# Kernel tuning notes

Hardware: AMD Instinct MI355X
Metric: run time of the kernel (lower is better)

Reference implementation:

```python
import jax, jax.numpy as jnp
import numpy as np

B, T1, T2, D, H, NL, DFF, NC = 4, 128, 128, 512, 4, 4, 2048, 5
SQRT2 = 1.4142135623730951


def _ln(x, w, b, eps=1e-12):
    m = jnp.mean(x, -1, keepdims=True)
    v = jnp.mean((x - m) ** 2, -1, keepdims=True)
    return w * (x - m) / jnp.sqrt(v + eps) + b


def _gelu(x):  # erf-based gelu, as in source
    return x * 0.5 * (1.0 + jax.lax.erf(x / SQRT2))


def _mha(x, wq, bq, wk, bk, wv, bv, wo, bo):
    b, t, d = x.shape
    dk = d // H
    q = (x @ wq + bq).reshape(b, t, H, dk).transpose(0, 2, 1, 3)
    k = (x @ wk + bk).reshape(b, t, H, dk).transpose(0, 2, 1, 3)
    v = (x @ wv + bv).reshape(b, t, H, dk).transpose(0, 2, 1, 3)
    p = jax.nn.softmax(jnp.einsum('bhqd,bhkd->bhqk', q, k) / jnp.sqrt(jnp.float32(dk)), -1)
    o = jnp.einsum('bhqk,bhkd->bhqd', p, v).transpose(0, 2, 1, 3).reshape(b, t, d)
    return o @ wo + bo


def _encode(x, pos_emb, pe_w, pe_b, Wq, bq, Wk, bk, Wv, bv, Wo, bo,
            ff1_w, ff1_b, ff2_w, ff2_b, lnin_w, lnin_b, lnout_w, lnout_b):
    t = x.shape[1]
    x = _ln(x + pos_emb[:t], pe_w, pe_b)  # PositionalEncoding (dropout=0 eval)
    for i in range(Wq.shape[0]):  # EncoderLayer x NL
        x = x + _mha(x, Wq[i], bq[i], Wk[i], bk[i], Wv[i], bv[i], Wo[i], bo[i])
        h = _ln(x, lnin_w[i], lnin_b[i])
        x = x + (_gelu(h @ ff1_w[i] + ff1_b[i]) @ ff2_w[i] + ff2_b[i])
        x = _ln(x, lnout_w[i], lnout_b[i])
    return x


def _forward(q_emb, a_emb, qa_relation, aq_relation, concept_emb, pos_emb, pe_w, pe_b,
             Wq, bq, Wk, bk, Wv, bv, Wo, bo, ff1_w, ff1_b, ff2_w, ff2_b,
             lnin_w, lnin_b, lnout_w, lnout_b, sim_Wq, sim_bq, sim_Wk, sim_bk, cls_w, cls_b):
    enc = lambda x: _encode(x, pos_emb, pe_w, pe_b, Wq, bq, Wk, bk, Wv, bv, Wo, bo,
                            ff1_w, ff1_b, ff2_w, ff2_b, lnin_w, lnin_b, lnout_w, lnout_b)
    qe = enc(q_emb)   # [B,T1,D]
    ae = enc(a_emb)   # [B,T2,D]
    # ConceptEncoding: relation one-hots -> concept embedding mix
    hL = qa_relation @ concept_emb   # [B,T1,T2,D]
    hR = aq_relation @ concept_emb   # [B,T2,T1,D]
    # SimAttn: note source uses fwK for BOTH key and value, so v == k exactly
    q = qe @ sim_Wq + sim_bq
    k = ae @ sim_Wk + sim_bk
    kR = jnp.transpose(k[:, :, None, :] + hR, (0, 2, 1, 3))  # [B,T1,T2,D]
    scores = jnp.sum((q[:, :, None, :] + hL) * kR, axis=-1)   # [B,T1,T2]
    p = jax.nn.softmax(scores, -1)
    # sharpening branch (default sharpening=True): re-softmax the attention probs
    p = jnp.clip(jax.nn.softmax(1000.0 * p, -1), 0.0, 1.0)
    # value path: v + hR transposed == kR since v == k
    x = jnp.einsum('bts,btsd->btd', p, kR)                    # [B,T1,D]
    return jnp.mean(x, 1) @ cls_w + cls_b                     # [B,3]


def setup_inputs() -> dict:
    key = jax.random.key(0)
    rk = lambda i: jax.random.fold_in(key, i)
    w = lambda i, shape: 0.02 * jax.random.normal(rk(i), shape, jnp.float32)
    z = lambda shape: jnp.zeros(shape, jnp.float32)
    o = lambda shape: jnp.ones(shape, jnp.float32)
    return {
        'q_emb': jax.random.normal(rk(0), (B, T1, D), jnp.float32),
        'a_emb': jax.random.normal(rk(1), (B, T2, D), jnp.float32),
        'qa_relation': jax.random.uniform(rk(2), (B, T1, T2, NC), jnp.float32),
        'aq_relation': jax.random.uniform(rk(3), (B, T2, T1, NC), jnp.float32),
        'concept_emb': w(4, (NC, D)),
        'pos_emb': w(5, (512, D)),
        'pe_w': o((D,)), 'pe_b': z((D,)),
        'Wq': w(6, (NL, D, D)), 'bq': z((NL, D)),
        'Wk': w(7, (NL, D, D)), 'bk': z((NL, D)),
        'Wv': w(8, (NL, D, D)), 'bv': z((NL, D)),
        'Wo': w(9, (NL, D, D)), 'bo': z((NL, D)),
        'ff1_w': w(10, (NL, D, DFF)), 'ff1_b': z((NL, DFF)),
        'ff2_w': w(11, (NL, DFF, D)), 'ff2_b': z((NL, D)),
        'lnin_w': o((NL, D)), 'lnin_b': z((NL, D)),
        'lnout_w': o((NL, D)), 'lnout_b': z((NL, D)),
        'sim_Wq': w(12, (D, D)), 'sim_bq': z((D,)),
        'sim_Wk': w(13, (D, D)), 'sim_bk': z((D,)),
        'cls_w': w(14, (D, 3)), 'cls_b': z((3,)),
    }


def reference(q_emb, a_emb, qa_relation, aq_relation, concept_emb, pos_emb, pe_w, pe_b,
              Wq, bq, Wk, bk, Wv, bv, Wo, bo, ff1_w, ff1_b, ff2_w, ff2_b,
              lnin_w, lnin_b, lnout_w, lnout_b, sim_Wq, sim_bq, sim_Wk, sim_bk, cls_w, cls_b):
    return _forward(q_emb, a_emb, qa_relation, aq_relation, concept_emb, pos_emb, pe_w, pe_b,
                    Wq, bq, Wk, bk, Wv, bv, Wo, bo, ff1_w, ff1_b, ff2_w, ff2_b,
                    lnin_w, lnin_b, lnout_w, lnout_b, sim_Wq, sim_bq, sim_Wk, sim_bk, cls_w, cls_b)
```

## Files before the change

kernel.cpp:

```cpp
#include <hip/hip_runtime.h>
#include <hip/hip_bf16.h>
#include <math.h>

typedef unsigned short u16;
typedef __attribute__((ext_vector_type(8))) short bf16x8;
typedef __attribute__((ext_vector_type(4))) float f32x4;

__device__ __forceinline__ float ldin(const void* p, size_t i, int isbf) {
  if (isbf) return __bfloat162float(((const __hip_bfloat16*)p)[i]);
  return ((const float*)p)[i];
}
__device__ __forceinline__ float bfu(u16 u) { return __builtin_bit_cast(float, (unsigned)u << 16); }
__device__ __forceinline__ u16 f2bf(float x) {
  unsigned u = __builtin_bit_cast(unsigned, x);
  unsigned r = u + 0x7FFFu + ((u >> 16) & 1u);
  return (u16)(r >> 16);
}

__device__ __forceinline__ float wave_sum(float v) {
#pragma unroll
  for (int o = 32; o > 0; o >>= 1) v += __shfl_down(v, o);
  return v;
}

__device__ __forceinline__ float block_sum(float v, float* sbuf) {
  int lane = threadIdx.x & 63;
  int wid = threadIdx.x >> 6;
#pragma unroll
  for (int o = 32; o > 0; o >>= 1) v += __shfl_down(v, o);
  __syncthreads();
  if (lane == 0) sbuf[wid] = v;
  __syncthreads();
  int nw = blockDim.x >> 6;
  if (wid == 0) {
    float r = (lane < nw) ? sbuf[lane] : 0.f;
#pragma unroll
    for (int o = 4; o > 0; o >>= 1) r += __shfl_down(r, o);
    if (lane == 0) sbuf[0] = r;
  }
  __syncthreads();
  return sbuf[0];
}

__device__ __forceinline__ float block_max(float v, float* sbuf) {
  int lane = threadIdx.x & 63;
  int wid = threadIdx.x >> 6;
#pragma unroll
  for (int o = 32; o > 0; o >>= 1) v = fmaxf(v, __shfl_down(v, o));
  __syncthreads();
  if (lane == 0) sbuf[wid] = v;
  __syncthreads();
  int nw = blockDim.x >> 6;
  if (wid == 0) {
    float r = (lane < nw) ? sbuf[lane] : -INFINITY;
#pragma unroll
    for (int o = 4; o > 0; o >>= 1) r = fmaxf(r, __shfl_down(r, o));
    if (lane == 0) sbuf[0] = r;
  }
  __syncthreads();
  return sbuf[0];
}

__global__ void flag_kernel(const void* pe_w, int* flag) {
  if (threadIdx.x == 0 && blockIdx.x == 0)
    *flag = (((const unsigned short*)pe_w)[0] != 0) ? 1 : 0;
}

__global__ void init_kernel(const void* pe_w, int* flag, float* Pbar, float* pabar) {
  int t = threadIdx.x;
  if (t == 0) *flag = (((const unsigned short*)pe_w)[0] != 0) ? 1 : 0;
  if (t < 512) Pbar[t] = 0.f;
  if (t < 20) pabar[t] = 0.f;
}


__global__ __launch_bounds__(256) void convT2(
    const void* __restrict__ S0, const void* __restrict__ S1,
    const void* __restrict__ S2, const void* __restrict__ S3,
    size_t srcStride, int K, int N, u16* __restrict__ Dh, u16* __restrict__ Dl,
    size_t layerStride, size_t tensorStride, int tmask, int lshift,
    const int* __restrict__ dflag) {
  const int isbf = *dflag;
  int z = blockIdx.z;
  int t = z & tmask, l = z >> lshift;
  const void* S = (t == 0) ? S0 : ((t == 1) ? S1 : ((t == 2) ? S2 : S3));
  size_t soff = (size_t)l * srcStride;
  size_t doff = (size_t)l * layerStride + (size_t)t * tensorStride;
  int n0 = blockIdx.x * 32, k0 = blockIdx.y * 32;
  __shared__ float tt[32][33];
  int tx = threadIdx.x & 31, ty = threadIdx.x >> 5;
#pragma unroll
  for (int j = 0; j < 4; ++j) {
    int r = ty + j * 8;
    tt[r][tx] = ldin(S, soff + (size_t)(k0 + r) * N + n0 + tx, isbf);
  }
  __syncthreads();
#pragma unroll
  for (int j = 0; j < 4; ++j) {
    int r = ty + j * 8;
    float v = tt[tx][r];
    u16 h = f2bf(v);
    u16 lo = f2bf(v - bfu(h));
    size_t o = doff + (size_t)(n0 + r) * K + k0 + tx;
    Dh[o] = h;
    Dl[o] = lo;
  }
}

__global__ __launch_bounds__(256) void gemm_hl(
    const u16* __restrict__ Ahp, const u16* __restrict__ Alp, int lda,
    const u16* __restrict__ Whp, const u16* __restrict__ Wlp, int ldw,
    const void* __restrict__ b0, const void* __restrict__ b1, const void* __restrict__ b2,
    size_t bo0, size_t bo1, size_t bo2, int bshift,
    float* __restrict__ C, u16* __restrict__ Chp, u16* __restrict__ Clp,
    u16* __restrict__ Vh, u16* __restrict__ Vl, int ldc,
    int K, int act, int mode, int ysplit, size_t wrowoff1,
    const int* __restrict__ dflag) {
  const int isbf = *dflag;
  __shared__ __align__(16) u16 sAh[64][72];
  __shared__ __align__(16) u16 sAl[64][72];
  __shared__ __align__(16) u16 sBh[64][72];
  __shared__ __align__(16) u16 sBl[64][72];

  int tid = threadIdx.x;
  int by = blockIdx.y;
  int row0 = by * 64, col0 = blockIdx.x * 64;
  int rsplit = (by >= ysplit);
  size_t wrow0 = (size_t)col0 + (rsplit ? wrowoff1 : 0);
  int Ksub = K / (int)gridDim.z;
  int kstart = (int)blockIdx.z * Ksub;
  int addbias = (blockIdx.z == 0);

  int wid = tid >> 6, lane = tid & 63, quad = lane >> 4, lm = lane & 15;
  int mrow = (wid & 1) * 32, ncol = (wid >> 1) * 32;

  f32x4 acc[2][2] = {};

  int sr = tid >> 2, sc = (tid & 3) * 16;

  for (int k0 = kstart; k0 < kstart + Ksub; k0 += 64) {
    const u16* p;
    p = Ahp + (size_t)(row0 + sr) * lda + k0 + sc;
    uint4 a0 = *(const uint4*)p, a1 = *(const uint4*)(p + 8);
    p = Alp + (size_t)(row0 + sr) * lda + k0 + sc;
    uint4 a2 = *(const uint4*)p, a3 = *(const uint4*)(p + 8);
    p = Whp + (wrow0 + sr) * (size_t)ldw + k0 + sc;
    uint4 w0 = *(const uint4*)p, w1 = *(const uint4*)(p + 8);
    p = Wlp + (wrow0 + sr) * (size_t)ldw + k0 + sc;
    uint4 w2 = *(const uint4*)p, w3 = *(const uint4*)(p + 8);
    __syncthreads();
    *(uint4*)&sAh[sr][sc] = a0; *(uint4*)&sAh[sr][sc + 8] = a1;
    *(uint4*)&sAl[sr][sc] = a2; *(uint4*)&sAl[sr][sc + 8] = a3;
    *(uint4*)&sBh[sr][sc] = w0; *(uint4*)&sBh[sr][sc + 8] = w1;
    *(uint4*)&sBl[sr][sc] = w2; *(uint4*)&sBl[sr][sc + 8] = w3;
    __syncthreads();
#pragma unroll
    for (int ks = 0; ks < 2; ++ks) {
      bf16x8 ah[2], al[2], wh[2], wl[2];
#pragma unroll
      for (int mi = 0; mi < 2; ++mi) {
        ah[mi] = *(const bf16x8*)&sAh[mrow + mi * 16 + lm][ks * 32 + quad * 8];
        al[mi] = *(const bf16x8*)&sAl[mrow + mi * 16 + lm][ks * 32 + quad * 8];
      }
#pragma unroll
      for (int ni = 0; ni < 2; ++ni) {
        wh[ni] = *(const bf16x8*)&sBh[ncol + ni * 16 + lm][ks * 32 + quad * 8];
        wl[ni] = *(const bf16x8*)&sBl[ncol + ni * 16 + lm][ks * 32 + quad * 8];
      }
#pragma unroll
      for (int mi = 0; mi < 2; ++mi)
#pragma unroll
        for (int ni = 0; ni < 2; ++ni) {
          acc[mi][ni] = __builtin_amdgcn_mfma_f32_16x16x32_bf16(ah[mi], wh[ni], acc[mi][ni], 0, 0, 0);
          acc[mi][ni] = __builtin_amdgcn_mfma_f32_16x16x32_bf16(al[mi], wh[ni], acc[mi][ni], 0, 0, 0);
          acc[mi][ni] = __builtin_amdgcn_mfma_f32_16x16x32_bf16(ah[mi], wl[ni], acc[mi][ni], 0, 0, 0);
        }
    }
  }
#pragma unroll
  for (int mi = 0; mi < 2; ++mi) {
#pragma unroll
    for (int ni = 0; ni < 2; ++ni) {
      int colg = col0 + ncol + ni * 16 + lm;
      const void* bp; size_t bo;
      if (rsplit) { bp = b1; bo = bo1 + colg; }
      else {
        int seg = colg >> bshift;
        bp = (seg == 0) ? b0 : ((seg == 1) ? b1 : b2);
        bo = (seg == 0) ? bo0 : ((seg == 1) ? bo1 : bo2);
        bo += (size_t)colg - ((size_t)seg << bshift);
      }
      float bv = addbias ? ldin(bp, bo, isbf) : 0.f;
#pragma unroll
      for (int r = 0; r < 4; ++r) {
        int rowg = row0 + mrow + mi * 16 + quad * 4 + r;
        float v = acc[mi][ni][r] + bv;
        if (act) v = v * 0.5f * (1.f + erff(v * 0.70710678118654752f));
        if (mode == 3 && colg >= 1024) {
          int gg = rowg >> 7;
          size_t o = ((size_t)(gg * 512) + (colg - 1024)) * 128 + (rowg & 127);
          u16 hh = f2bf(v); Vh[o] = hh; Vl[o] = f2bf(v - bfu(hh));
        } else {
          size_t o = (size_t)rowg * ldc + colg;
          if (mode == 0) C[o] = v;
          else if (mode == 1) atomicAdd(&C[o], v);
          else { u16 hh = f2bf(v); Chp[o] = hh; Clp[o] = f2bf(v - bfu(hh)); }
        }
      }
    }
  }
}

__global__ __launch_bounds__(256) void attn_mfma(
    const u16* __restrict__ Qh, const u16* __restrict__ Ql,
    const u16* __restrict__ Vth, const u16* __restrict__ Vtl,
    u16* __restrict__ Oh, u16* __restrict__ Ol) {
  int tq = blockIdx.x & 3;
  int h = (blockIdx.x >> 2) & 3;
  int g = blockIdx.x >> 4;
  int tid = threadIdx.x;
  int w = tid >> 6, lane = tid & 63, quad = lane >> 4, lm = lane & 15;
  __shared__ float S[32][132];

  f32x4 sacc[2][2] = {};
#pragma unroll
  for (int ks = 0; ks < 4; ++ks) {
    bf16x8 qh[2], ql[2];
#pragma unroll
    for (int mi = 0; mi < 2; ++mi) {
      size_t qi = (size_t)(g * 128 + tq * 32 + mi * 16 + lm) * 1536 + h * 128 + ks * 32 + quad * 8;
      qh[mi] = *(const bf16x8*)(Qh + qi);
      ql[mi] = *(const bf16x8*)(Ql + qi);
    }
#pragma unroll
    for (int ni = 0; ni < 2; ++ni) {
      size_t kix = (size_t)(g * 128 + w * 32 + ni * 16 + lm) * 1536 + 512 + h * 128 + ks * 32 + quad * 8;
      bf16x8 kh = *(const bf16x8*)(Qh + kix);
      bf16x8 kl = *(const bf16x8*)(Ql + kix);
#pragma unroll
      for (int mi = 0; mi < 2; ++mi) {
        sacc[mi][ni] = __builtin_amdgcn_mfma_f32_16x16x32_bf16(qh[mi], kh, sacc[mi][ni], 0, 0, 0);
        sacc[mi][ni] = __builtin_amdgcn_mfma_f32_16x16x32_bf16(ql[mi], kh, sacc[mi][ni], 0, 0, 0);
        sacc[mi][ni] = __builtin_amdgcn_mfma_f32_16x16x32_bf16(qh[mi], kl, sacc[mi][ni], 0, 0, 0);
      }
    }
  }
  const float scale = 0.08838834764831845f;
#pragma unroll
  for (int mi = 0; mi < 2; ++mi)
#pragma unroll
    for (int ni = 0; ni < 2; ++ni)
#pragma unroll
      for (int r = 0; r < 4; ++r)
        S[mi * 16 + quad * 4 + r][w * 32 + ni * 16 + lm] = sacc[mi][ni][r] * scale;
  __syncthreads();

  {
    int row = tid >> 3, j = tid & 7;
    float* sp = &S[row][j * 16];
// ... 98 lines not shown
  u16 h1 = f2bf(r1); oh[o1] = h1; ol[o1] = f2bf(r1 - bfu(h1));
}

__global__ __launch_bounds__(256) void ln2(
    const float* __restrict__ in, float* __restrict__ outf,
    u16* __restrict__ oh, u16* __restrict__ ol,
    const void* __restrict__ w, const void* __restrict__ b, size_t wboff,
    const int* __restrict__ dflag) {
  const int isbf = *dflag;
  const int D = 512;
  int row = blockIdx.x;
  __shared__ float sbuf[8];
  int i0 = threadIdx.x, i1 = threadIdx.x + 256;
  float v0 = in[(size_t)row * D + i0];
  float v1 = in[(size_t)row * D + i1];
  float mean = block_sum(v0 + v1, sbuf) / 512.f;
  float d0 = v0 - mean, d1 = v1 - mean;
  float var = block_sum(d0 * d0 + d1 * d1, sbuf) / 512.f;
  float inv = 1.0f / sqrtf(var + 1e-12f);
  float r0 = ldin(w, wboff + i0, isbf) * d0 * inv + ldin(b, wboff + i0, isbf);
  float r1 = ldin(w, wboff + i1, isbf) * d1 * inv + ldin(b, wboff + i1, isbf);
  size_t o0 = (size_t)row * D + i0, o1 = (size_t)row * D + i1;
  if (outf) { outf[o0] = r0; outf[o1] = r1; }
  u16 h0 = f2bf(r0); oh[o0] = h0; ol[o0] = f2bf(r0 - bfu(h0));
  u16 h1 = f2bf(r1); oh[o1] = h1; ol[o1] = f2bf(r1 - bfu(h1));
}

__global__ __launch_bounds__(64) void projgram(const float* __restrict__ qkb,
                                               const void* __restrict__ ce,
                                               float* __restrict__ ck, float* __restrict__ G,
                                               const int* __restrict__ dflag) {
  const int isbf = *dflag;
  if (blockIdx.x < 1024) {
    int row = blockIdx.x;
#pragma unroll
    for (int c = 0; c < 5; ++c) {
      float acc = 0.f;
      for (int d = threadIdx.x; d < 512; d += 64)
        acc = fmaf(qkb[(size_t)row * 512 + d], ldin(ce, (size_t)c * 512 + d, isbf), acc);
      acc = wave_sum(acc);
      if (threadIdx.x == 0) ck[row * 5 + c] = acc;
    }
  } else {
    int i = blockIdx.x - 1024;
    int c = i / 5, c2 = i % 5;
    float acc = 0.f;
    for (int d = threadIdx.x; d < 512; d += 64)
      acc = fmaf(ldin(ce, (size_t)c * 512 + d, isbf), ldin(ce, (size_t)c2 * 512 + d, isbf), acc);
    acc = wave_sum(acc);
    if (threadIdx.x == 0) G[i] = acc;
  }
}

__global__ __launch_bounds__(128) void scores_acc(
    const float* __restrict__ qkb, const void* __restrict__ qa, const void* __restrict__ aq,
    const float* __restrict__ ck, const float* __restrict__ G,
    float* __restrict__ Pbar, float* __restrict__ pabar, const int* __restrict__ dflag) {
  const int isbf = *dflag;
  const int T1 = 128, T2 = 128, D = 512, NC = 5;
  int t = blockIdx.x & 127;
  int b = blockIdx.x >> 7;
  int s = threadIdx.x;
  const float* q = qkb;
  const float* k = qkb + (size_t)512 * 512;
  __shared__ float qs[512];
  __shared__ float Gs[25];
  __shared__ float qcs[5];
  __shared__ float sbuf[8];
  for (int i = threadIdx.x; i < D; i += 128) qs[i] = q[(size_t)(b * T1 + t) * D + i];
  if (threadIdx.x < NC * NC) Gs[threadIdx.x] = G[threadIdx.x];
  if (threadIdx.x < NC) qcs[threadIdx.x] = ck[(size_t)(b * T1 + t) * NC + threadIdx.x];
  __syncthreads();
  const float* krow = k + (size_t)(b * T2 + s) * D;
  float sc = 0.f;
#pragma unroll 4
  for (int d = 0; d < 512; d += 4) {
    float4 kv4 = *(const float4*)(krow + d);
    sc = fmaf(qs[d], kv4.x, sc);
    sc = fmaf(qs[d + 1], kv4.y, sc);
    sc = fmaf(qs[d + 2], kv4.z, sc);
    sc = fmaf(qs[d + 3], kv4.w, sc);
  }
  float qav[5], aqv[5];
#pragma unroll
  for (int c = 0; c < 5; ++c) {
    qav[c] = ldin(qa, (size_t)((b * T1 + t) * T2 + s) * NC + c, isbf);
    aqv[c] = ldin(aq, (size_t)((b * T2 + s) * T1 + t) * NC + c, isbf);
  }
#pragma unroll
  for (int c = 0; c < 5; ++c) {
    sc = fmaf(aqv[c], qcs[c], sc);
    sc = fmaf(qav[c], ck[(size_t)(512 + b * T2 + s) * NC + c], sc);
#pragma unroll
    for (int c2 = 0; c2 < 5; ++c2) sc = fmaf(qav[c] * Gs[c * 5 + c2], aqv[c2], sc);
  }
  float mx = block_max(sc, sbuf);
  float e = expf(sc - mx);
  float ssum = block_sum(e, sbuf);
  float p = e / ssum;
  float mx2 = block_max(p, sbuf);
  float e2 = expf(1000.f * (p - mx2));
  float s2 = block_sum(e2, sbuf);
  float pf = fminf(fmaxf(e2 / s2, 0.f), 1.f);
  atomicAdd(&Pbar[b * 128 + s], pf);
#pragma unroll
  for (int c = 0; c < 5; ++c) {
    float pc = block_sum(pf * aqv[c], sbuf);
    if (threadIdx.x == 0) atomicAdd(&pabar[b * 5 + c], pc);
  }
}

__global__ __launch_bounds__(512) void meancls(
    const float* __restrict__ qkb, const float* __restrict__ Pbar, const float* __restrict__ pabar,
    const void* __restrict__ ce, const void* __restrict__ clsw, const void* __restrict__ clsb,
    void* __restrict__ out, const int* __restrict__ dflag) {
  const int isbf = *dflag;
  int b = blockIdx.x;
  int d = threadIdx.x;
  __shared__ float Ps[128];
  __shared__ float pas[5];
  __shared__ float xm[512];
  __shared__ float sbuf[8];
  if (d < 128) Ps[d] = Pbar[b * 128 + d];
  if (d < 5) pas[d] = pabar[b * 5 + d];
  __syncthreads();
  const float* k = qkb + (size_t)(512 + b * 128) * 512 + d;
  float acc = 0.f;
  for (int s = 0; s < 128; ++s) acc = fmaf(Ps[s], k[(size_t)s * 512], acc);
#pragma unroll
  for (int c = 0; c < 5; ++c) acc = fmaf(pas[c], ldin(ce, (size_t)c * 512 + d, isbf), acc);
  acc *= (1.f / 128.f);
  xm[d] = acc;
  __syncthreads();
  for (int j = 0; j < 3; ++j) {
    float v = block_sum(xm[d] * ldin(clsw, (size_t)d * 3 + j, isbf), sbuf);
    if (d == 0) {
      float val = v + ldin(clsb, j, isbf);
      if (isbf) ((u16*)out)[b * 3 + j] = f2bf(val);
      else ((float*)out)[b * 3 + j] = val;
    }
    __syncthreads();
  }
}


__global__ __launch_bounds__(256) void gemm_mfma(
    const float* __restrict__ A, const void* __restrict__ W, size_t woff,
    const void* __restrict__ bias, size_t boff,
    float* __restrict__ C, int M, int N, int K, int act, int addto,
    const int* __restrict__ dflag) {
  const int isbf = *dflag;
  __shared__ __align__(16) u16 Ah[64][40];
  __shared__ __align__(16) u16 Al[64][40];
  __shared__ __align__(16) u16 Wh[64][40];
  __shared__ __align__(16) u16 Wl[64][40];
  int tid = threadIdx.x;
  int row0 = blockIdx.y * 64, col0 = blockIdx.x * 64;
  int wid = tid >> 6, lane = tid & 63;
  int quad = lane >> 4, lm = lane & 15;
  int mrow = (wid & 1) * 32, ncol = (wid >> 1) * 32;
  f32x4 acc[2][2] = {};
  int ar = tid >> 2, akc = (tid & 3) * 8;
  int bk = tid >> 3, bn0 = (tid & 7) * 8;
  for (int k0 = 0; k0 < K; k0 += 32) {
    const float* ap = A + (size_t)(row0 + ar) * K + k0 + akc;
    float av[8];
    *(float4*)(av) = *(const float4*)ap;
    *(float4*)(av + 4) = *(const float4*)(ap + 4);
    unsigned hp[4], lp[4];
#pragma unroll
    for (int j = 0; j < 4; ++j) {
      u16 h0 = f2bf(av[2 * j]);
      u16 h1 = f2bf(av[2 * j + 1]);
      u16 l0 = f2bf(av[2 * j] - bfu(h0));
      u16 l1 = f2bf(av[2 * j + 1] - bfu(h1));
      hp[j] = (unsigned)h0 | ((unsigned)h1 << 16);
      lp[j] = (unsigned)l0 | ((unsigned)l1 << 16);
    }
// ... 210 lines not shown
  __shared__ float ps[128];
  __shared__ float pav[5];
  if (threadIdx.x < T2) ps[threadIdx.x] = p[(size_t)(b * T1 + t) * T2 + threadIdx.x];
  if (threadIdx.x < NC) pav[threadIdx.x] = pa[(b * T1 + t) * NC + threadIdx.x];
  __syncthreads();
  float acc = 0.f;
  for (int s = 0; s < 128; ++s) acc = fmaf(ps[s], k[(size_t)(b * T2 + s) * D + d], acc);
#pragma unroll
  for (int c = 0; c < 5; ++c) acc = fmaf(pav[c], ldin(ce, (size_t)c * D + d, isbf), acc);
  x[(size_t)(b * T1 + t) * D + d] = acc;
}

__global__ __launch_bounds__(512) void mean_kernel(const float* __restrict__ x, float* __restrict__ xm,
                                                   int T, int D) {
  int b = blockIdx.x;
  int d = threadIdx.x;
  float acc = 0.f;
  for (int t = 0; t < T; ++t) acc += x[(size_t)(b * T + t) * D + d];
  xm[(size_t)b * D + d] = acc / (float)T;
}

__global__ __launch_bounds__(64) void cls_kernel(const float* __restrict__ xm,
                                                 const void* __restrict__ w,
                                                 const void* __restrict__ bias,
                                                 void* __restrict__ out, int D, int NO,
                                                 const int* __restrict__ dflag) {
  const int isbf = *dflag;
  int j = blockIdx.x % NO;
  int b = blockIdx.x / NO;
  float acc = 0.f;
  for (int d = threadIdx.x; d < D; d += 64)
    acc = fmaf(xm[(size_t)b * D + d], ldin(w, (size_t)d * NO + j, isbf), acc);
  acc = wave_sum(acc);
  if (threadIdx.x == 0) {
    float val = acc + ldin(bias, j, isbf);
    if (isbf) ((__hip_bfloat16*)out)[b * NO + j] = __float2bfloat16(val);
    else ((float*)out)[b * NO + j] = val;
  }
}

extern "C" void kernel_launch(void* const* d_in, const int* in_sizes, int n_in,
                              void* d_out, int out_size, void* d_ws, size_t ws_size,
                              hipStream_t stream) {
  const int B = 4, T = 128, D = 512, H = 4, NL = 4, DFF = 2048, NC = 5;
  const void *q_emb = d_in[0], *a_emb = d_in[1], *qa = d_in[2], *aqr = d_in[3],
             *ce = d_in[4], *pos = d_in[5], *pe_w = d_in[6], *pe_b = d_in[7],
             *Wq = d_in[8], *bq = d_in[9], *Wk = d_in[10], *bk = d_in[11],
             *Wv = d_in[12], *bv = d_in[13], *Wo = d_in[14], *bo = d_in[15],
             *ff1w = d_in[16], *ff1b = d_in[17], *ff2w = d_in[18], *ff2b = d_in[19],
             *lnin_w = d_in[20], *lnin_b = d_in[21], *lnout_w = d_in[22], *lnout_b = d_in[23],
             *simWq = d_in[24], *simbq = d_in[25], *simWk = d_in[26], *simbk = d_in[27],
             *clsw = d_in[28], *clsb = d_in[29];

  const size_t REQ = 79000000ull;
  if (ws_size >= REQ) {
    char* base = (char*)d_ws;
    float* x = (float*)(base + 0);
    u16* xch = (u16*)(base + 2097152);
    u16* xcl = (u16*)(base + 3145728);
    u16* qkvh = (u16*)(base + 4194304);
    u16* qkvl = (u16*)(base + 7340032);
    u16* ffch = (u16*)(base + 10485760);
    u16* ffcl = (u16*)(base + 14680064);
    u16* Vth = (u16*)(base + 18874368);
    u16* Vtl = (u16*)(base + 19922944);
    float* qkb = (float*)(base + 20971520);
    float* ck = (float*)(base + 25165824);
    float* Gbuf = (float*)(base + 25186304);
    float* Pbar = (float*)(base + 25190400);
    float* pabar = (float*)(base + 25192448);
    int* dflag = (int*)(base + 25196544);
    u16* wh = (u16*)(base + 26214400);
    u16* wl = (u16*)(base + 52428800);

    init_kernel<<<1, 512, 0, stream>>>(pe_w, dflag, Pbar, pabar);
    convT2<<<dim3(16, 16, 16), 256, 0, stream>>>(Wq, Wk, Wv, Wo, 262144, 512, 512,
                                                 wh, wl, 3145728, 262144, 3, 2, dflag);
    convT2<<<dim3(64, 16, 4), 256, 0, stream>>>(ff1w, ff1w, ff1w, ff1w, 1048576, 512, 2048,
                                                wh + 1048576, wl + 1048576, 3145728, 0, 0, 0, dflag);
    convT2<<<dim3(16, 64, 4), 256, 0, stream>>>(ff2w, ff2w, ff2w, ff2w, 1048576, 2048, 512,
                                                wh + 2097152, wl + 2097152, 3145728, 0, 0, 0, dflag);
    convT2<<<dim3(16, 16, 2), 256, 0, stream>>>(simWq, simWk, simWk, simWk, 0, 512, 512,
                                                wh + 12582912, wl + 12582912, 0, 262144, 1, 1, dflag);

    emb_ln2<<<1024, 256, 0, stream>>>(q_emb, a_emb, pos, pe_w, pe_b, x, xch, xcl, dflag);

    for (int l = 0; l < NL; ++l) {
      size_t wbase = (size_t)l * 3145728, bD = (size_t)l * D;
      gemm_hl<<<dim3(24, 16, 1), 256, 0, stream>>>(xch, xcl, 512, wh + wbase, wl + wbase, 512,
                                                   bq, bk, bv, bD, bD, bD, 9,
                                                   nullptr, qkvh, qkvl, Vth, Vtl, 1536,
                                                   512, 0, 3, 9999, 0, dflag);
      attn_mfma<<<128, 256, 0, stream>>>(qkvh, qkvl, Vth, Vtl, xch, xcl);
      gemm_hl<<<dim3(8, 16, 2), 256, 0, stream>>>(xch, xcl, 512, wh + wbase + 786432,
                                                  wl + wbase + 786432, 512,
                                                  bo, bo, bo, bD, bD, bD, 9,
                                                  x, nullptr, nullptr, nullptr, nullptr, 512,
                                                  512, 0, 1, 9999, 0, dflag);
      ln2<<<1024, 256, 0, stream>>>(x, nullptr, xch, xcl, lnin_w, lnin_b, bD, dflag);
      gemm_hl<<<dim3(32, 16, 1), 256, 0, stream>>>(xch, xcl, 512, wh + wbase + 1048576,
                                                   wl + wbase + 1048576, 512,
                                                   ff1b, ff1b, ff1b,
                                                   (size_t)l * DFF, (size_t)l * DFF, (size_t)l * DFF, 11,
                                                   nullptr, ffch, ffcl, nullptr, nullptr, 2048,
                                                   512, 1, 2, 9999, 0, dflag);
      gemm_hl<<<dim3(8, 16, 2), 256, 0, stream>>>(ffch, ffcl, 2048, wh + wbase + 2097152,
                                                  wl + wbase + 2097152, 2048,
                                                  ff2b, ff2b, ff2b, bD, bD, bD, 9,
                                                  x, nullptr, nullptr, nullptr, nullptr, 512,
                                                  2048, 0, 1, 9999, 0, dflag);
      ln2<<<1024, 256, 0, stream>>>(x, x, xch, xcl, lnout_w, lnout_b, bD, dflag);
    }

    gemm_hl<<<dim3(8, 16, 1), 256, 0, stream>>>(xch, xcl, 512, wh + 12582912, wl + 12582912, 512,
                                                simbq, simbk, simbk, 0, 0, 0, 9,
                                                qkb, nullptr, nullptr, nullptr, nullptr, 512,
                                                512, 0, 0, 8, 512, dflag);
    projgram<<<1049, 64, 0, stream>>>(qkb, ce, ck, Gbuf, dflag);
    scores_acc<<<512, 128, 0, stream>>>(qkb, qa, aqr, ck, Gbuf, Pbar, pabar, dflag);
    meancls<<<4, 512, 0, stream>>>(qkb, Pbar, pabar, ce, clsw, clsb, d_out, dflag);
    return;
  }

  float* ws = (float*)d_ws;
  const size_t S = (size_t)512 * 512;
  float* qe = ws;
  float* ae = ws + S;
  float* hb = ws + 2 * S;
  float* rb = ws + 3 * S;
  float* qb = rb;
  float* kb = rb + S;
  float* vb = rb + 2 * S;
  float* ob = rb + 3 * S;
  float* ffb = rb;
  float* pbuf = rb + 2 * S;
  float* pabuf = pbuf + 65536;
  float* qcbuf = pabuf + 2560;
  float* kcbuf = qcbuf + 2560;
  float* Gbuf = kcbuf + 2560;
  float* xmean = Gbuf + 32;
  float* xsim = rb + 3 * S;
  int* dflag = (int*)(ws + 7 * S);

  const int M = B * T;
  dim3 gD(8, 8), gF1(32, 8), gF2(8, 8);

  flag_kernel<<<1, 64, 0, stream>>>(pe_w, dflag);
  for (int e = 0; e < 2; ++e) {
    float* x = (e == 0) ? qe : ae;
    const void* emb = (e == 0) ? q_emb : a_emb;
    emb_ln_kernel<<<M, 256, 0, stream>>>(emb, pos, pe_w, pe_b, x, T, D, dflag);
    for (int l = 0; l < NL; ++l) {
      size_t wDD = (size_t)l * D * D, bD = (size_t)l * D;
      gemm_mfma<<<gD, 256, 0, stream>>>(x, Wq, wDD, bq, bD, qb, M, D, D, 0, 0, dflag);
      gemm_mfma<<<gD, 256, 0, stream>>>(x, Wk, wDD, bk, bD, kb, M, D, D, 0, 0, dflag);
      gemm_mfma<<<gD, 256, 0, stream>>>(x, Wv, wDD, bv, bD, vb, M, D, D, 0, 0, dflag);
      attn_kernel<<<B * H * T, 128, 0, stream>>>(qb, kb, vb, ob, B, H, T, D / H);
      gemm_mfma<<<gD, 256, 0, stream>>>(ob, Wo, wDD, bo, bD, x, M, D, D, 0, 1, dflag);
      ln_kernel<<<M, 256, 0, stream>>>(x, hb, lnin_w, lnin_b, bD, D, dflag);
      gemm_mfma<<<gF1, 256, 0, stream>>>(hb, ff1w, (size_t)l * D * DFF, ff1b, (size_t)l * DFF,
                                         ffb, M, DFF, D, 1, 0, dflag);
      gemm_mfma<<<gF2, 256, 0, stream>>>(ffb, ff2w, (size_t)l * DFF * D, ff2b, bD,
                                         x, M, D, DFF, 0, 1, dflag);
      ln_kernel<<<M, 256, 0, stream>>>(x, x, lnout_w, lnout_b, bD, D, dflag);
    }
  }
  gemm_mfma<<<gD, 256, 0, stream>>>(qe, simWq, 0, simbq, 0, qb, M, D, D, 0, 0, dflag);
  gemm_mfma<<<gD, 256, 0, stream>>>(ae, simWk, 0, simbk, 0, kb, M, D, D, 0, 0, dflag);
  proj_ce_kernel<<<M, 64, 0, stream>>>(qb, ce, qcbuf, D, NC, dflag);
  proj_ce_kernel<<<M, 64, 0, stream>>>(kb, ce, kcbuf, D, NC, dflag);
  gram_kernel<<<NC * NC, 64, 0, stream>>>(ce, Gbuf, D, NC, dflag);
  sim_scores_kernel<<<B * T, 128, 0, stream>>>(qb, kb, qa, aqr, qcbuf, kcbuf, Gbuf, pbuf, pabuf,
                                               B, T, T, D, NC, dflag);
// ... 5 lines not shown
```

Measured before the change: 606.2 us.

## Compute sim-attention scores with MFMA and move reductions into meancls

Replaces the per-row scalar scores_acc kernel with a prep_rel kernel that precomputes the relation terms and a scores_mfma kernel. That kernel computes the q·k scores with split-bf16 MFMA, adds the relation terms, does the double softmax in registers and writes the full P matrix. The sim projection GEMM gains a mode that also emits hi/lo bf16 copies for the MFMA path. Pbar/pabar atomics and the init kernel are dropped, and meancls now reduces P itself. The trade-off is that scores_mfma launches only 16 blocks, plus an extra kernel and more workspace traffic.

```diff
diff --git a/kernel.cpp b/kernel.cpp
--- a/kernel.cpp
+++ b/kernel.cpp
@@ -64,13 +64,6 @@
 __global__ void flag_kernel(const void* pe_w, int* flag) {
   if (threadIdx.x == 0 && blockIdx.x == 0)
     *flag = (((const unsigned short*)pe_w)[0] != 0) ? 1 : 0;
-}
-
-__global__ void init_kernel(const void* pe_w, int* flag, float* Pbar, float* pabar) {
-  int t = threadIdx.x;
-  if (t == 0) *flag = (((const unsigned short*)pe_w)[0] != 0) ? 1 : 0;
-  if (t < 512) Pbar[t] = 0.f;
-  if (t < 20) pabar[t] = 0.f;
 }
 
 
@@ -204,7 +197,12 @@
           size_t o = (size_t)rowg * ldc + colg;
           if (mode == 0) C[o] = v;
           else if (mode == 1) atomicAdd(&C[o], v);
-          else { u16 hh = f2bf(v); Chp[o] = hh; Clp[o] = f2bf(v - bfu(hh)); }
+          else if (mode == 4) {
+            C[o] = v;
+            u16 hh = f2bf(v); Chp[o] = hh; Clp[o] = f2bf(v - bfu(hh));
+          } else {
+            u16 hh = f2bf(v); Chp[o] = hh; Clp[o] = f2bf(v - bfu(hh));
+          }
         }
       }
     }
@@ -409,78 +407,184 @@
   }
 }
 
-__global__ __launch_bounds__(128) void scores_acc(
-    const float* __restrict__ qkb, const void* __restrict__ qa, const void* __restrict__ aq,
-    const float* __restrict__ ck, const float* __restrict__ G,
-    float* __restrict__ Pbar, float* __restrict__ pabar, const int* __restrict__ dflag) {
-  const int isbf = *dflag;
-  const int T1 = 128, T2 = 128, D = 512, NC = 5;
-  int t = blockIdx.x & 127;
-  int b = blockIdx.x >> 7;
-  int s = threadIdx.x;
-  const float* q = qkb;
-  const float* k = qkb + (size_t)512 * 512;
-  __shared__ float qs[512];
+__global__ __launch_bounds__(256) void prep_rel(
+    const void* __restrict__ aq, const float* __restrict__ ck, const float* __restrict__ G,
+    float* __restrict__ mT, float* __restrict__ nT, const int* __restrict__ dflag) {
+  const int isbf = *dflag;
+  int bx = blockIdx.x;
+  int t0 = (bx & 3) * 32;
+  int s0 = ((bx >> 2) & 3) * 32;
+  int b = bx >> 4;
+  int tid = threadIdx.x;
+  __shared__ float aqs[32][164];
   __shared__ float Gs[25];
-  __shared__ float qcs[5];
-  __shared__ float sbuf[8];
-  for (int i = threadIdx.x; i < D; i += 128) qs[i] = q[(size_t)(b * T1 + t) * D + i];
-  if (threadIdx.x < NC * NC) Gs[threadIdx.x] = G[threadIdx.x];
-  if (threadIdx.x < NC) qcs[threadIdx.x] = ck[(size_t)(b * T1 + t) * NC + threadIdx.x];
-  __syncthreads();
-  const float* krow = k + (size_t)(b * T2 + s) * D;
-  float sc = 0.f;
-#pragma unroll 4
-  for (int d = 0; d < 512; d += 4) {
-    float4 kv4 = *(const float4*)(krow + d);
-    sc = fmaf(qs[d], kv4.x, sc);
-    sc = fmaf(qs[d + 1], kv4.y, sc);
-    sc = fmaf(qs[d + 2], kv4.z, sc);
-    sc = fmaf(qs[d + 3], kv4.w, sc);
-  }
-  float qav[5], aqv[5];
-#pragma unroll
-  for (int c = 0; c < 5; ++c) {
-    qav[c] = ldin(qa, (size_t)((b * T1 + t) * T2 + s) * NC + c, isbf);
-    aqv[c] = ldin(aq, (size_t)((b * T2 + s) * T1 + t) * NC + c, isbf);
-  }
-#pragma unroll
-  for (int c = 0; c < 5; ++c) {
-    sc = fmaf(aqv[c], qcs[c], sc);
-    sc = fmaf(qav[c], ck[(size_t)(512 + b * T2 + s) * NC + c], sc);
-#pragma unroll
-    for (int c2 = 0; c2 < 5; ++c2) sc = fmaf(qav[c] * Gs[c * 5 + c2], aqv[c2], sc);
-  }
-  float mx = block_max(sc, sbuf);
-  float e = expf(sc - mx);
-  float ssum = block_sum(e, sbuf);
-  float p = e / ssum;
-  float mx2 = block_max(p, sbuf);
-  float e2 = expf(1000.f * (p - mx2));
-  float s2 = block_sum(e2, sbuf);
-  float pf = fminf(fmaxf(e2 / s2, 0.f), 1.f);
-  atomicAdd(&Pbar[b * 128 + s], pf);
-#pragma unroll
-  for (int c = 0; c < 5; ++c) {
-    float pc = block_sum(pf * aqv[c], sbuf);
-    if (threadIdx.x == 0) atomicAdd(&pabar[b * 5 + c], pc);
+  __shared__ float kcs[32][5];
+  __shared__ float qcs[32][5];
+  for (int i = tid; i < 5120; i += 256) {
+    int s = i / 160, r = i % 160;
+    aqs[s][r] = ldin(aq, ((size_t)(b * 128 + s0 + s) * 128 + t0) * 5 + r, isbf);
+  }
+  if (tid < 25) Gs[tid] = G[tid];
+  for (int i = tid; i < 160; i += 256)
+    kcs[i / 5][i % 5] = ck[(size_t)(512 + b * 128 + s0 + i / 5) * 5 + i % 5];
+  for (int i = tid; i < 160; i += 256)
+    qcs[i / 5][i % 5] = ck[(size_t)(b * 128 + t0 + i / 5) * 5 + i % 5];
+  __syncthreads();
+  for (int i = tid; i < 5120; i += 256) {
+    int t = i / 160, j = i % 160, s = j / 5, c = j % 5;
+    float ga = 0.f;
+#pragma unroll
+    for (int c2 = 0; c2 < 5; ++c2) ga = fmaf(Gs[c * 5 + c2], aqs[s][t * 5 + c2], ga);
+    mT[((size_t)(b * 128 + t0 + t) * 128 + s0 + s) * 5 + c] = kcs[s][c] + ga;
+  }
+  for (int i = tid; i < 1024; i += 256) {
+    int t = i >> 5, s = i & 31;
+    float n = 0.f;
+#pragma unroll
+    for (int c = 0; c < 5; ++c) n = fmaf(aqs[s][t * 5 + c], qcs[t][c], n);
+    nT[(size_t)(b * 128 + t0 + t) * 128 + s0 + s] = n;
+  }
+}
+
+__global__ __launch_bounds__(256) void scores_mfma(
+    const u16* __restrict__ Qh, const u16* __restrict__ Ql,
+    const void* __restrict__ qa, const float* __restrict__ mT, const float* __restrict__ nT,
+    float* __restrict__ P, const int* __restrict__ dflag) {
+  const int isbf = *dflag;
+  int tq = blockIdx.x & 3;
+  int b = blockIdx.x >> 2;
+  int tid = threadIdx.x;
+  int w = tid >> 6, lane = tid & 63, quad = lane >> 4, lm = lane & 15;
+  __shared__ float S[32][132];
+
+  f32x4 sacc[2][2] = {};
+#pragma unroll
+  for (int ks = 0; ks < 16; ++ks) {
+    bf16x8 qh[2], ql[2];
+#pragma unroll
+    for (int mi = 0; mi < 2; ++mi) {
+      size_t qi = (size_t)(b * 128 + tq * 32 + mi * 16 + lm) * 512 + ks * 32 + quad * 8;
+      qh[mi] = *(const bf16x8*)(Qh + qi);
+      ql[mi] = *(const bf16x8*)(Ql + qi);
+    }
+#pragma unroll
+    for (int ni = 0; ni < 2; ++ni) {
+      size_t ki = (size_t)(512 + b * 128 + w * 32 + ni * 16 + lm) * 512 + ks * 32 + quad * 8;
+      bf16x8 kh = *(const bf16x8*)(Qh + ki);
+      bf16x8 kl = *(const bf16x8*)(Ql + ki);
+#pragma unroll
+      for (int mi = 0; mi < 2; ++mi) {
+        sacc[mi][ni] = __builtin_amdgcn_mfma_f32_16x16x32_bf16(qh[mi], kh, sacc[mi][ni], 0, 0, 0);
+        sacc[mi][ni] = __builtin_amdgcn_mfma_f32_16x16x32_bf16(ql[mi], kh, sacc[mi][ni], 0, 0, 0);
+        sacc[mi][ni] = __builtin_amdgcn_mfma_f32_16x16x32_bf16(qh[mi], kl, sacc[mi][ni], 0, 0, 0);
+      }
+    }
+  }
+#pragma unroll
+  for (int mi = 0; mi < 2; ++mi)
+#pragma unroll
+    for (int ni = 0; ni < 2; ++ni)
+#pragma unroll
+      for (int r = 0; r < 4; ++r)
+        S[mi * 16 + quad * 4 + r][w * 32 + ni * 16 + lm] = sacc[mi][ni][r];
+  __syncthreads();
+
+  {
+    int t = tid >> 3;
+    int s0 = (tid & 7) * 16;
+    size_t gt = (size_t)(b * 128 + tq * 32 + t);
+    for (int s = s0; s < s0 + 16; ++s) {
+      size_t o = gt * 128 + s;
+      float r = nT[o];
+      size_t o5 = o * 5;
+#pragma unroll
+      for (int c = 0; c < 5; ++c) r = fmaf(ldin(qa, o5 + c, isbf), mT[o5 + c], r);
+      S[t][s] += r;
+    }
+  }
+  __syncthreads();
+
+  {
+    int row = tid >> 3, j = tid & 7;
+    float* sp = &S[row][j * 16];
+    float v[16];
+    *(float4*)(v) = *(float4*)(sp);
+    *(float4*)(v + 4) = *(float4*)(sp + 4);
+    *(float4*)(v + 8) = *(float4*)(sp + 8);
+    *(float4*)(v + 12) = *(float4*)(sp + 12);
+    float mx = v[0];
+#pragma unroll
+    for (int i = 1; i < 16; ++i) mx = fmaxf(mx, v[i]);
+    mx = fmaxf(mx, __shfl_xor(mx, 1));
+    mx = fmaxf(mx, __shfl_xor(mx, 2));
+    mx = fmaxf(mx, __shfl_xor(mx, 4));
+    float sum = 0.f;
+#pragma unroll
+    for (int i = 0; i < 16; ++i) { v[i] = expf(v[i] - mx); sum += v[i]; }
+    sum += __shfl_xor(sum, 1);
+    sum += __shfl_xor(sum, 2);
+    sum += __shfl_xor(sum, 4);
+    float inv = 1.f / sum;
+#pragma unroll
+    for (int i = 0; i < 16; ++i) v[i] *= inv;
+    float mx2 = v[0];
+#pragma unroll
+    for (int i = 1; i < 16; ++i) mx2 = fmaxf(mx2, v[i]);
+    mx2 = fmaxf(mx2, __shfl_xor(mx2, 1));
+    mx2 = fmaxf(mx2, __shfl_xor(mx2, 2));
+    mx2 = fmaxf(mx2, __shfl_xor(mx2, 4));
+    float sum2 = 0.f;
+#pragma unroll
+    for (int i = 0; i < 16; ++i) { v[i] = expf(1000.f * (v[i] - mx2)); sum2 += v[i]; }
+    sum2 += __shfl_xor(sum2, 1);
+    sum2 += __shfl_xor(sum2, 2);
+    sum2 += __shfl_xor(sum2, 4);
+    float inv2 = 1.f / sum2;
+#pragma unroll
+    for (int i = 0; i < 16; ++i) v[i] = fminf(fmaxf(v[i] * inv2, 0.f), 1.f);
+    float* pp = P + ((size_t)(b * 128 + tq * 32 + row)) * 128 + j * 16;
+    *(float4*)(pp) = *(float4*)(v);
+    *(float4*)(pp + 4) = *(float4*)(v + 4);
+    *(float4*)(pp + 8) = *(float4*)(v + 8);
+    *(float4*)(pp + 12) = *(float4*)(v + 12);
   }
 }
 
 __global__ __launch_bounds__(512) void meancls(
-    const float* __restrict__ qkb, const float* __restrict__ Pbar, const float* __restrict__ pabar,
+    const float* __restrict__ qkb, const float* __restrict__ P, const void* __restrict__ aq,
     const void* __restrict__ ce, const void* __restrict__ clsw, const void* __restrict__ clsb,
     void* __restrict__ out, const int* __restrict__ dflag) {
   const int isbf = *dflag;
   int b = blockIdx.x;
-  int d = threadIdx.x;
+  int tid = threadIdx.x;
   __shared__ float Ps[128];
   __shared__ float pas[5];
   __shared__ float xm[512];
   __shared__ float sbuf[8];
-  if (d < 128) Ps[d] = Pbar[b * 128 + d];
-  if (d < 5) pas[d] = pabar[b * 5 + d];
-  __syncthreads();
+  if (tid < 5) pas[tid] = 0.f;
+  __syncthreads();
+  {
+    int s = tid >> 2, jj = tid & 3;
+    float pac[5] = {0.f, 0.f, 0.f, 0.f, 0.f};
+    for (int t = jj * 32; t < jj * 32 + 32; ++t) {
+      float pv = P[((size_t)(b * 128 + t)) * 128 + s];
+      size_t ao = ((size_t)(b * 128 + s) * 128 + t) * 5;
+#pragma unroll
+      for (int c = 0; c < 5; ++c) pac[c] = fmaf(pv, ldin(aq, ao + c, isbf), pac[c]);
+    }
+#pragma unroll
+    for (int c = 0; c < 5; ++c) {
+      float v = wave_sum(pac[c]);
+      if ((tid & 63) == 0) atomicAdd(&pas[c], v);
+    }
+  }
+  if (tid < 128) {
+    float a = 0.f;
+    for (int t = 0; t < 128; ++t) a += P[((size_t)(b * 128 + t)) * 128 + tid];
+    Ps[tid] = a;
+  }
+  __syncthreads();
+  int d = tid;
   const float* k = qkb + (size_t)(512 + b * 128) * 512 + d;
   float acc = 0.f;
   for (int s = 0; s < 128; ++s) acc = fmaf(Ps[s], k[(size_t)s * 512], acc);
@@ -797,7 +901,7 @@
              *simWq = d_in[24], *simbq = d_in[25], *simWk = d_in[26], *simbk = d_in[27],
              *clsw = d_in[28], *clsb = d_in[29];
 
-  const size_t REQ = 79000000ull;
+  const size_t REQ = 82000000ull;
   if (ws_size >= REQ) {
     char* base = (char*)d_ws;
     float* x = (float*)(base + 0);
@@ -810,15 +914,18 @@
     u16* Vth = (u16*)(base + 18874368);
     u16* Vtl = (u16*)(base + 19922944);
     float* qkb = (float*)(base + 20971520);
+    u16* qsh = (u16*)(base + 23068672);
+    u16* qsl = (u16*)(base + 24117248);
     float* ck = (float*)(base + 25165824);
     float* Gbuf = (float*)(base + 25186304);
-    float* Pbar = (float*)(base + 25190400);
-    float* pabar = (float*)(base + 25192448);
     int* dflag = (int*)(base + 25196544);
     u16* wh = (u16*)(base + 26214400);
     u16* wl = (u16*)(base + 52428800);
-
-    init_kernel<<<1, 512, 0, stream>>>(pe_w, dflag, Pbar, pabar);
+    float* P = (float*)(base + 79691776);
+    float* mT = (float*)(base + 79953920);
+    float* nT = (float*)(base + 81264640);
+
+    flag_kernel<<<1, 64, 0, stream>>>(pe_w, dflag);
     convT2<<<dim3(16, 16, 16), 256, 0, stream>>>(Wq, Wk, Wv, Wo, 262144, 512, 512,
                                                  wh, wl, 3145728, 262144, 3, 2, dflag);
     convT2<<<dim3(64, 16, 4), 256, 0, stream>>>(ff1w, ff1w, ff1w, ff1w, 1048576, 512, 2048,
@@ -859,11 +966,12 @@
 
     gemm_hl<<<dim3(8, 16, 1), 256, 0, stream>>>(xch, xcl, 512, wh + 12582912, wl + 12582912, 512,
                                                 simbq, simbk, simbk, 0, 0, 0, 9,
-                                                qkb, nullptr, nullptr, nullptr, nullptr, 512,
-                                                512, 0, 0, 8, 512, dflag);
+                                                qkb, qsh, qsl, nullptr, nullptr, 512,
+                                                512, 0, 4, 8, 512, dflag);
     projgram<<<1049, 64, 0, stream>>>(qkb, ce, ck, Gbuf, dflag);
-    scores_acc<<<512, 128, 0, stream>>>(qkb, qa, aqr, ck, Gbuf, Pbar, pabar, dflag);
-    meancls<<<4, 512, 0, stream>>>(qkb, Pbar, pabar, ce, clsw, clsb, d_out, dflag);
+    prep_rel<<<64, 256, 0, stream>>>(aqr, ck, Gbuf, mT, nT, dflag);
+    scores_mfma<<<16, 256, 0, stream>>>(qsh, qsl, qa, mT, nT, P, dflag);
+    meancls<<<4, 512, 0, stream>>>(qkb, P, aqr, ce, clsw, clsb, d_out, dflag);
     return;
   }
 
```

Result: slower. 664.0 us (+9.5%).

## Compute sim-attention scores with MFMA GEMM and split relation/softmax stages

Applied to the files above, without the earlier changes.

The per-row scalar q·k dot products in scores_acc are replaced by a batched split-bf16 MFMA GEMM (new mode 5, split-K with atomic accumulation into a zeroed score buffer). The sim projection also emits hi/lo bf16 copies for this purpose. The relation-bias terms move into a separate tiled prep kernel that stages aq in shared memory. Softmax now writes a transposed probability matrix, and a new reduction kernel computes Pbar and pabar, removing the per-element atomics. This adds three launches and more workspace traffic in exchange for using matrix cores and coalesced accesses.

```diff
diff --git a/kernel.cpp b/kernel.cpp
--- a/kernel.cpp
+++ b/kernel.cpp
@@ -66,11 +66,14 @@
     *flag = (((const unsigned short*)pe_w)[0] != 0) ? 1 : 0;
 }
 
-__global__ void init_kernel(const void* pe_w, int* flag, float* Pbar, float* pabar) {
-  int t = threadIdx.x;
-  if (t == 0) *flag = (((const unsigned short*)pe_w)[0] != 0) ? 1 : 0;
-  if (t < 512) Pbar[t] = 0.f;
-  if (t < 20) pabar[t] = 0.f;
+__global__ __launch_bounds__(256) void init_kernel(const void* pe_w, int* flag,
+                                                   float* Sbuf, float* pabar) {
+  int i = blockIdx.x * 256 + threadIdx.x;
+  ((float4*)Sbuf)[i] = make_float4(0.f, 0.f, 0.f, 0.f);
+  if (blockIdx.x == 0) {
+    if (threadIdx.x == 0) *flag = (((const unsigned short*)pe_w)[0] != 0) ? 1 : 0;
+    if (threadIdx.x < 20) pabar[threadIdx.x] = 0.f;
+  }
 }
 
 
@@ -127,9 +130,10 @@
   int row0 = by * 64, col0 = blockIdx.x * 64;
   int rsplit = (by >= ysplit);
   size_t wrow0 = (size_t)col0 + (rsplit ? wrowoff1 : 0);
+  if (mode == 5) wrow0 = wrowoff1 + (size_t)(by >> 1) * 128 + col0;
   int Ksub = K / (int)gridDim.z;
   int kstart = (int)blockIdx.z * Ksub;
-  int addbias = (blockIdx.z == 0);
+  int addbias = (blockIdx.z == 0) && (mode != 5);
 
   int wid = tid >> 6, lane = tid & 63, quad = lane >> 4, lm = lane & 15;
   int mrow = (wid & 1) * 32, ncol = (wid >> 1) * 32;
@@ -182,15 +186,18 @@
 #pragma unroll
     for (int ni = 0; ni < 2; ++ni) {
       int colg = col0 + ncol + ni * 16 + lm;
-      const void* bp; size_t bo;
-      if (rsplit) { bp = b1; bo = bo1 + colg; }
-      else {
-        int seg = colg >> bshift;
-        bp = (seg == 0) ? b0 : ((seg == 1) ? b1 : b2);
-        bo = (seg == 0) ? bo0 : ((seg == 1) ? bo1 : bo2);
-        bo += (size_t)colg - ((size_t)seg << bshift);
+      float bv = 0.f;
+      if (addbias) {
+        const void* bp; size_t bo;
+        if (rsplit) { bp = b1; bo = bo1 + colg; }
+        else {
+          int seg = colg >> bshift;
+          bp = (seg == 0) ? b0 : ((seg == 1) ? b1 : b2);
+          bo = (seg == 0) ? bo0 : ((seg == 1) ? bo1 : bo2);
+          bo += (size_t)colg - ((size_t)seg << bshift);
+        }
+        bv = ldin(bp, bo, isbf);
       }
-      float bv = addbias ? ldin(bp, bo, isbf) : 0.f;
 #pragma unroll
       for (int r = 0; r < 4; ++r) {
         int rowg = row0 + mrow + mi * 16 + quad * 4 + r;
@@ -203,8 +210,13 @@
         } else {
           size_t o = (size_t)rowg * ldc + colg;
           if (mode == 0) C[o] = v;
-          else if (mode == 1) atomicAdd(&C[o], v);
-          else { u16 hh = f2bf(v); Chp[o] = hh; Clp[o] = f2bf(v - bfu(hh)); }
+          else if (mode == 1 || mode == 5) atomicAdd(&C[o], v);
+          else if (mode == 4) {
+            C[o] = v;
+            u16 hh = f2bf(v); Chp[o] = hh; Clp[o] = f2bf(v - bfu(hh));
+          } else {
+            u16 hh = f2bf(v); Chp[o] = hh; Clp[o] = f2bf(v - bfu(hh));
+          }
         }
       }
     }
@@ -409,48 +421,55 @@
   }
 }
 
-__global__ __launch_bounds__(128) void scores_acc(
-    const float* __restrict__ qkb, const void* __restrict__ qa, const void* __restrict__ aq,
+__global__ __launch_bounds__(256) void prep_rel(
+    const void* __restrict__ aq, const void* __restrict__ qa,
     const float* __restrict__ ck, const float* __restrict__ G,
-    float* __restrict__ Pbar, float* __restrict__ pabar, const int* __restrict__ dflag) {
-  const int isbf = *dflag;
-  const int T1 = 128, T2 = 128, D = 512, NC = 5;
-  int t = blockIdx.x & 127;
-  int b = blockIdx.x >> 7;
+    float* __restrict__ R, const int* __restrict__ dflag) {
+  const int isbf = *dflag;
+  int bx = blockIdx.x;
+  int t0 = (bx & 3) * 32;
+  int s0 = ((bx >> 2) & 3) * 32;
+  int b = bx >> 4;
+  int tid = threadIdx.x;
+  __shared__ float aqs[32][164];
+  __shared__ float Gs[25];
+  __shared__ float kcs[32][5];
+  __shared__ float qcs[32][5];
+  for (int i = tid; i < 5120; i += 256) {
+    int s = i / 160, r = i % 160;
+    aqs[s][r] = ldin(aq, ((size_t)(b * 128 + s0 + s) * 128 + t0) * 5 + r, isbf);
+  }
+  if (tid < 25) Gs[tid] = G[tid];
+  for (int i = tid; i < 160; i += 256)
+    kcs[i / 5][i % 5] = ck[(size_t)(512 + b * 128 + s0 + i / 5) * 5 + i % 5];
+  for (int i = tid; i < 160; i += 256)
+    qcs[i / 5][i % 5] = ck[(size_t)(b * 128 + t0 + i / 5) * 5 + i % 5];
+  __syncthreads();
+  for (int i = tid; i < 1024; i += 256) {
+    int t = i >> 5, s = i & 31;
+    size_t qoff = ((size_t)(b * 128 + t0 + t) * 128 + s0 + s) * 5;
+    float r = 0.f;
+#pragma unroll
+    for (int c = 0; c < 5; ++c) {
+      float ga = 0.f;
+#pragma unroll
+      for (int c2 = 0; c2 < 5; ++c2) ga = fmaf(Gs[c * 5 + c2], aqs[s][t * 5 + c2], ga);
+      r = fmaf(ldin(qa, qoff + c, isbf), kcs[s][c] + ga, r);
+      r = fmaf(aqs[s][t * 5 + c], qcs[t][c], r);
+    }
+    R[(size_t)(b * 128 + t0 + t) * 128 + s0 + s] = r;
+  }
+}
+
+__global__ __launch_bounds__(128) void softmax_rel(
+    const float* __restrict__ Sbuf, const float* __restrict__ R,
+    float* __restrict__ PT) {
+  int row = blockIdx.x;
+  int b = row >> 7, t = row & 127;
   int s = threadIdx.x;
-  const float* q = qkb;
-  const float* k = qkb + (size_t)512 * 512;
-  __shared__ float qs[512];
-  __shared__ float Gs[25];
-  __shared__ float qcs[5];
   __shared__ float sbuf[8];
-  for (int i = threadIdx.x; i < D; i += 128) qs[i] = q[(size_t)(b * T1 + t) * D + i];
-  if (threadIdx.x < NC * NC) Gs[threadIdx.x] = G[threadIdx.x];
-  if (threadIdx.x < NC) qcs[threadIdx.x] = ck[(size_t)(b * T1 + t) * NC + threadIdx.x];
-  __syncthreads();
-  const float* krow = k + (size_t)(b * T2 + s) * D;
-  float sc = 0.f;
-#pragma unroll 4
-  for (int d = 0; d < 512; d += 4) {
-    float4 kv4 = *(const float4*)(krow + d);
-    sc = fmaf(qs[d], kv4.x, sc);
-    sc = fmaf(qs[d + 1], kv4.y, sc);
-    sc = fmaf(qs[d + 2], kv4.z, sc);
-    sc = fmaf(qs[d + 3], kv4.w, sc);
-  }
-  float qav[5], aqv[5];
-#pragma unroll
-  for (int c = 0; c < 5; ++c) {
-    qav[c] = ldin(qa, (size_t)((b * T1 + t) * T2 + s) * NC + c, isbf);
-    aqv[c] = ldin(aq, (size_t)((b * T2 + s) * T1 + t) * NC + c, isbf);
-  }
-#pragma unroll
-  for (int c = 0; c < 5; ++c) {
-    sc = fmaf(aqv[c], qcs[c], sc);
-    sc = fmaf(qav[c], ck[(size_t)(512 + b * T2 + s) * NC + c], sc);
-#pragma unroll
-    for (int c2 = 0; c2 < 5; ++c2) sc = fmaf(qav[c] * Gs[c * 5 + c2], aqv[c2], sc);
-  }
+  size_t o = (size_t)row * 128 + s;
+  float sc = Sbuf[o] + R[o];
   float mx = block_max(sc, sbuf);
   float e = expf(sc - mx);
   float ssum = block_sum(e, sbuf);
@@ -459,11 +478,32 @@
   float e2 = expf(1000.f * (p - mx2));
   float s2 = block_sum(e2, sbuf);
   float pf = fminf(fmaxf(e2 / s2, 0.f), 1.f);
-  atomicAdd(&Pbar[b * 128 + s], pf);
-#pragma unroll
-  for (int c = 0; c < 5; ++c) {
-    float pc = block_sum(pf * aqv[c], sbuf);
-    if (threadIdx.x == 0) atomicAdd(&pabar[b * 5 + c], pc);
+  PT[(size_t)(b * 128 + s) * 128 + t] = pf;
+}
+
+__global__ __launch_bounds__(64) void pbar2(
+    const float* __restrict__ PT, const void* __restrict__ aq,
+    float* __restrict__ Pbar, float* __restrict__ pabar,
+    const int* __restrict__ dflag) {
+  const int isbf = *dflag;
+  int bs = blockIdx.x;
+  int b = bs >> 7;
+  int lane = threadIdx.x;
+  int t0 = lane * 2;
+  float2 pt = *(const float2*)(PT + (size_t)bs * 128 + t0);
+  size_t ao = ((size_t)bs * 128 + t0) * 5;
+  float psum = pt.x + pt.y;
+  float pac[5];
+#pragma unroll
+  for (int c = 0; c < 5; ++c)
+    pac[c] = pt.x * ldin(aq, ao + c, isbf) + pt.y * ldin(aq, ao + 5 + c, isbf);
+  psum = wave_sum(psum);
+#pragma unroll
+  for (int c = 0; c < 5; ++c) pac[c] = wave_sum(pac[c]);
+  if (lane == 0) {
+    Pbar[bs] = psum;
+#pragma unroll
+    for (int c = 0; c < 5; ++c) atomicAdd(&pabar[b * 5 + c], pac[c]);
   }
 }
 
@@ -473,14 +513,15 @@
     void* __restrict__ out, const int* __restrict__ dflag) {
   const int isbf = *dflag;
   int b = blockIdx.x;
-  int d = threadIdx.x;
+  int tid = threadIdx.x;
   __shared__ float Ps[128];
   __shared__ float pas[5];
   __shared__ float xm[512];
   __shared__ float sbuf[8];
-  if (d < 128) Ps[d] = Pbar[b * 128 + d];
-  if (d < 5) pas[d] = pabar[b * 5 + d];
-  __syncthreads();
+  if (tid < 128) Ps[tid] = Pbar[b * 128 + tid];
+  if (tid < 5) pas[tid] = pabar[b * 5 + tid];
+  __syncthreads();
+  int d = tid;
   const float* k = qkb + (size_t)(512 + b * 128) * 512 + d;
   float acc = 0.f;
   for (int s = 0; s < 128; ++s) acc = fmaf(Ps[s], k[(size_t)s * 512], acc);
@@ -797,7 +838,7 @@
              *simWq = d_in[24], *simbq = d_in[25], *simWk = d_in[26], *simbk = d_in[27],
              *clsw = d_in[28], *clsb = d_in[29];
 
-  const size_t REQ = 79000000ull;
+  const size_t REQ = 83000000ull;
   if (ws_size >= REQ) {
     char* base = (char*)d_ws;
     float* x = (float*)(base + 0);
@@ -810,6 +851,8 @@
     u16* Vth = (u16*)(base + 18874368);
     u16* Vtl = (u16*)(base + 19922944);
     float* qkb = (float*)(base + 20971520);
+    u16* qsh = (u16*)(base + 23068672);
+    u16* qsl = (u16*)(base + 24117248);
     float* ck = (float*)(base + 25165824);
     float* Gbuf = (float*)(base + 25186304);
     float* Pbar = (float*)(base + 25190400);
@@ -817,8 +860,11 @@
     int* dflag = (int*)(base + 25196544);
     u16* wh = (u16*)(base + 26214400);
     u16* wl = (u16*)(base + 52428800);
-
-    init_kernel<<<1, 512, 0, stream>>>(pe_w, dflag, Pbar, pabar);
+    float* Sbuf = (float*)(base + 79691776);
+    float* R = (float*)(base + 79953920);
+    float* PT = (float*)(base + 80216064);
+
+    init_kernel<<<64, 256, 0, stream>>>(pe_w, dflag, Sbuf, pabar);
     convT2<<<dim3(16, 16, 16), 256, 0, stream>>>(Wq, Wk, Wv, Wo, 262144, 512, 512,
                                                  wh, wl, 3145728, 262144, 3, 2, dflag);
     convT2<<<dim3(64, 16, 4), 256, 0, stream>>>(ff1w, ff1w, ff1w, ff1w, 1048576, 512, 2048,
@@ -859,10 +905,16 @@
 
     gemm_hl<<<dim3(8, 16, 1), 256, 0, stream>>>(xch, xcl, 512, wh + 12582912, wl + 12582912, 512,
                                                 simbq, simbk, simbk, 0, 0, 0, 9,
-                                                qkb, nullptr, nullptr, nullptr, nullptr, 512,
-                                                512, 0, 0, 8, 512, dflag);
+                                                qkb, qsh, qsl, nullptr, nullptr, 512,
+                                                512, 0, 4, 8, 512, dflag);
     projgram<<<1049, 64, 0, stream>>>(qkb, ce, ck, Gbuf, dflag);
-    scores_acc<<<512, 128, 0, stream>>>(qkb, qa, aqr, ck, Gbuf, Pbar, pabar, dflag);
+    prep_rel<<<64, 256, 0, stream>>>(aqr, qa, ck, Gbuf, R, dflag);
+    gemm_hl<<<dim3(2, 8, 4), 256, 0, stream>>>(qsh, qsl, 512, qsh, qsl, 512,
+                                               nullptr, nullptr, nullptr, 0, 0, 0, 9,
+                                               Sbuf, nullptr, nullptr, nullptr, nullptr, 128,
+                                               512, 0, 5, 9999, 512, dflag);
+    softmax_rel<<<512, 128, 0, stream>>>(Sbuf, R, PT);
+    pbar2<<<512, 64, 0, stream>>>(PT, aqr, Pbar, pabar, dflag);
     meancls<<<4, 512, 0, stream>>>(qkb, Pbar, pabar, ce, clsw, clsb, d_out, dflag);
     return;
   }
```

After: 627.9 us. 1.04x slower.
